# Optimization experiments

Measured on AMD Instinct MI355X. Metric: run time of the kernel, lower is better.

Reference implementation:

```python
import jax, jax.numpy as jnp
import numpy as np

H, N, L, B = 256, 64, 8192, 16   # d_model, d_state, l_max, batch
NH = N // 2                      # complex conjugate-pair halves (S4D convention)


def setup_inputs() -> dict:
    key = jax.random.key(0)
    ks = jax.random.split(key, 8)
    x = jax.random.normal(ks[0], (L, B, H), jnp.float32)
    # dt log-uniform in [1e-3, 1e-1] as in S4
    log_dt = jax.random.uniform(ks[1], (H,), jnp.float32) * (np.log(0.1) - np.log(0.001)) + np.log(0.001)
    # S4D-Lin initialization: A = -1/2 + i*pi*n
    A_real = jnp.log(0.5) * jnp.ones((H, NH), jnp.float32)            # log(-Re A)
    A_imag = np.pi * jnp.tile(jnp.arange(NH, dtype=jnp.float32), (H, 1))
    # 2 kernel channels for bidirectional
    C_real = jax.random.normal(ks[2], (2, H, NH), jnp.float32) * (0.5 ** 0.5)
    C_imag = jax.random.normal(ks[3], (2, H, NH), jnp.float32) * (0.5 ** 0.5)
    D = jax.random.normal(ks[4], (H,), jnp.float32)
    # position-wise output linear with GLU: H -> 2H, then glu over channel dim
    W_out = jax.random.normal(ks[5], (2 * H, H), jnp.float32) / np.sqrt(H)
    b_out = jnp.zeros((2 * H,), jnp.float32)
    return dict(x=x, log_dt=log_dt, A_real=A_real, A_imag=A_imag,
                C_real=C_real, C_imag=C_imag, D=D, W_out=W_out, b_out=b_out)


def _s4d_kernel(log_dt, A_real, A_imag, C_real, C_imag, length):
    """ZOH-discretized diagonal SSM kernel via Vandermonde. Returns (2, H, length) real."""
    dt = jnp.exp(log_dt)[:, None]                      # (H, 1)
    A = -jnp.exp(A_real) + 1j * A_imag                 # (H, NH)
    C = C_real + 1j * C_imag                           # (2, H, NH)
    dtA = A * dt                                       # (H, NH)
    Cd = C * (jnp.expm1(dtA) / A)                      # discretized C, (2, H, NH)
    # Vandermonde matrix exp(dtA * l) for l in [0, length)
    V = jnp.exp(dtA[:, :, None] * jnp.arange(length, dtype=jnp.float32))  # (H, NH, length)
    K = 2.0 * jnp.einsum('chn,hnl->chl', Cd, V).real   # (2, H, length)
    return K


def reference(x, log_dt, A_real, A_imag, C_real, C_imag, D, W_out, b_out):
    u = jnp.transpose(x, (1, 2, 0))                    # (B, H, L) -- TFTest transpose [1,2,0]
    Lq = u.shape[-1]
    n = 2 * Lq
    K = _s4d_kernel(log_dt, A_real, A_imag, C_real, C_imag, Lq)  # (2, H, L)
    # bidirectional: forward kernel padded right, flipped backward kernel padded left
    k = jnp.pad(K[0], ((0, 0), (0, Lq))) + jnp.pad(K[1][:, ::-1], ((0, 0), (Lq, 0)))  # (H, 2L)
    k_f = jnp.fft.rfft(k, n=n)                         # (H, n//2+1)
    u_f = jnp.fft.rfft(u, n=n)                         # (B, H, n//2+1)
    y = jnp.fft.irfft(u_f * k_f, n=n)[..., :Lq]        # (B, H, L)
    y = y + u * D[:, None]                             # skip connection
    y = jax.nn.gelu(y)
    z = jnp.einsum('oh,bhl->bol', W_out, y) + b_out[:, None]  # (B, 2H, L)
    out = z[:, :H] * jax.nn.sigmoid(z[:, H:])          # GLU over channel dim
    return out                                         # (B, H, L)
```

## Files before the change

kernel.cpp:

```cpp
#include <hip/hip_runtime.h>
#include <hip/hip_bf16.h>
#include <math.h>

#define HH  256
#define NHD 32
#define LL  8192
#define BB  16
#define HN  (HH*NHD)
#define BH  (BB*HH)
#define LC  256
#define NG  (LL/LC)
#define NINST (BB*NG)

typedef __attribute__((ext_vector_type(8))) short short8;
typedef __attribute__((ext_vector_type(4))) float floatx4;

__device__ __forceinline__ unsigned short f2bf(float f) {
  unsigned u = __float_as_uint(f);
  unsigned r = (u + 0x7FFF + ((u >> 16) & 1)) >> 16;
  return (unsigned short)r;
}
__device__ __forceinline__ float bf2f(unsigned short s) {
  return __uint_as_float((unsigned)s << 16);
}
__device__ __forceinline__ unsigned packbf2(float a, float b) {
  return (unsigned)f2bf(a) | ((unsigned)f2bf(b) << 16);
}
__device__ __forceinline__ float gelu_t(float y) {
  float y2 = y * y;
  float arg = 1.5957691216f * fmaf(0.044715f * y2, y, y);
  return y / (1.f + __expf(-arg));
}

__global__ void precomp_kernel(const float* __restrict__ log_dt,
                               const float* __restrict__ A_real,
                               const float* __restrict__ A_imag,
                               const float* __restrict__ C_real,
                               const float* __restrict__ C_imag,
                               float* __restrict__ P) {
  int i = blockIdx.x * blockDim.x + threadIdx.x;
  if (i >= HN) return;
  int h = i >> 5;
  double dt  = exp((double)log_dt[h]);
  double Are = -exp((double)A_real[i]);
  double Aim = (double)A_imag[i];
  double ar = Are * dt, ai = Aim * dt;
  double ea = exp(ar);
  double wr = ea * cos(ai), wi = ea * sin(ai);
  double em_r = wr - 1.0, em_i = wi;
  double den = Are * Are + Aim * Aim;
  double rr = (em_r * Are + em_i * Aim) / den;
  double ri = (em_i * Are - em_r * Aim) / den;
  P[0*HN + i] = (float)wr;
  P[1*HN + i] = (float)wi;
  {
    double cr = (double)C_real[i], ci = (double)C_imag[i];
    P[2*HN + i] = (float)(2.0 * (cr * rr - ci * ri));
    P[3*HN + i] = (float)(2.0 * (cr * ri + ci * rr));
  }
  {
    double cr = (double)C_real[HN + i], ci = (double)C_imag[HN + i];
    P[4*HN + i] = (float)(2.0 * (cr * rr - ci * ri));
    P[5*HN + i] = (float)(2.0 * (cr * ri + ci * rr));
  }
  {
    double arL = ar * (double)LC, aiL = ai * (double)LC;
    double eaL = exp(arL);
    P[6*HN + i] = (float)(eaL * cos(aiL));
    P[7*HN + i] = (float)(eaL * sin(aiL));
  }
  P[8*HN + i] = (float)ar;
  P[9*HN + i] = (float)ai;
}

__global__ __launch_bounds__(256) void wt_frag_kernel(const float* __restrict__ W,
                                                      unsigned short* __restrict__ Wf) {
  int og = blockIdx.x;
  #pragma unroll
  for (int i = 0; i < 2; ++i) {
    int j = i * 256 + threadIdx.x;
    int ks = j >> 6, ln = (j >> 2) & 15, lg = j & 3;
    const float* src = W + (size_t)(og * 16 + ln) * 256 + ks * 32 + lg * 8;
    short8 vv;
    #pragma unroll
    for (int e = 0; e < 8; ++e) vv[e] = (short)f2bf(src[e]);
    ((short8*)Wf)[og * 512 + j] = vv;
  }
}

__global__ __launch_bounds__(256) void kprep_kernel(const float* __restrict__ P,
                                                    float* __restrict__ Kf,
                                                    float* __restrict__ Kb) {
  int i = blockIdx.x * 256 + threadIdx.x;
  int d = i & 255, h = i >> 8;
  float fd = (float)d;
  float sf = 0.f, sb = 0.f;
  #pragma unroll 4
  for (int n = 0; n < NHD; ++n) {
    int j = h * NHD + n;
    float m  = __expf(fd * P[8*HN + j]);
    float ph = fd * P[9*HN + j];
    float cs = cosf(ph), sn = sinf(ph);
    float re = m * cs, im = m * sn;
    sf += P[2*HN + j] * re - P[3*HN + j] * im;
    sb += P[4*HN + j] * re - P[5*HN + j] * im;
  }
  Kf[i] = sf;
  Kb[i] = sb;
}

__global__ __launch_bounds__(256) void tprep_kernel(const float* __restrict__ Kf,
                                                    const float* __restrict__ Kb,
                                                    const float* __restrict__ Dv,
                                                    unsigned short* __restrict__ T) {
  int h = blockIdx.x, tt = blockIdx.y;
  const float* kf = Kf + h * 256;
  const float* kb = Kb + h * 256;
  float dh = Dv[h];
  short8* out = (short8*)T;
  #pragma unroll
  for (int i = 0; i < 2; ++i) {
    int j = i * 256 + threadIdx.x;
    int ks = j >> 6, ln = (j >> 2) & 15, lg = j & 3;
    int t = tt * 16 + ln;
    short8 vv;
    #pragma unroll
    for (int e = 0; e < 8; ++e) {
      int s = ks * 32 + lg * 8 + e;
      int d = t - s;
      float v = (d > 0) ? kf[d] : ((d < 0) ? kb[-d - 1] : (kf[0] + dh));
      vv[e] = (short)f2bf(v);
    }
    out[(size_t)(h * 16 + tt) * 512 + j] = vv;
  }
}

__global__ __launch_bounds__(256) void eprep_kernel(const float* __restrict__ P,
                                                    unsigned short* __restrict__ E) {
  int h = blockIdx.x, tt = blockIdx.y;
  int j = threadIdx.x;
  int ks = j >> 6, ln = (j >> 2) & 15, lg = j & 3;
  int t = tt * 16 + ln;
  int k0 = ks * 32 + lg * 8;
  short8 vv;
  if (k0 < 64) {
    float d = (float)(t + 1);
    #pragma unroll
    for (int q = 0; q < 4; ++q) {
      int n = (k0 >> 1) + q;
      int idx = h * NHD + n;
      float m  = __expf(d * P[8*HN + idx]);
      float ph = d * P[9*HN + idx];
      float re = m * cosf(ph), im = m * sinf(ph);
      float cr = P[2*HN + idx], ci = P[3*HN + idx];
      float zr = cr * re - ci * im;
      float zi = cr * im + ci * re;
      vv[2*q]   = (short)f2bf(zr);
      vv[2*q+1] = (short)f2bf(-zi);
    }
  } else {
    float d = (float)(LC - 1 - t);
    #pragma unroll
    for (int q = 0; q < 4; ++q) {
      int n = ((k0 - 64) >> 1) + q;
      int idx = h * NHD + n;
      float m  = __expf(d * P[8*HN + idx]);
      float ph = d * P[9*HN + idx];
      float re = m * cosf(ph), im = m * sinf(ph);
      float cr = P[4*HN + idx], ci = P[5*HN + idx];
      float zr = cr * re - ci * im;
      float zi = cr * im + ci * re;
      vv[2*q]   = (short)f2bf(zr);
      vv[2*q+1] = (short)f2bf(-zi);
    }
  }
  ((short8*)E)[(size_t)(h * 16 + tt) * 256 + j] = vv;
}

__global__ __launch_bounds__(256) void vprep_kernel(const float* __restrict__ P,
                                                    unsigned short* __restrict__ V) {
  int h = blockIdx.x, mt = blockIdx.y;
  #pragma unroll
  for (int i = 0; i < 2; ++i) {
    int j = i * 256 + threadIdx.x;
    int ks = j >> 6, ln = (j >> 2) & 15, lg = j & 3;
    int row = mt * 16 + ln;
    int dir = row >> 6, nc = row & 63;
    int n = nc >> 1, comp = nc & 1;
    int idx = h * NHD + n;
    float arn = P[8*HN + idx], ain = P[9*HN + idx];
    short8 vv;
    #pragma unroll
    for (int e = 0; e < 8; ++e) {
      int s = ks * 32 + lg * 8 + e;
      float d = (float)(dir ? s : (LC - 1 - s));
      float m = __expf(d * arn);
      float ph = d * ain;
      float v = m * (comp ? sinf(ph) : cosf(ph));
      vv[e] = (short)f2bf(v);
    }
    ((short8*)V)[(size_t)(h * 8 + mt) * 512 + j] = vv;
  }
}

__global__ __launch_bounds__(256) void transpose_kernel(const float* __restrict__ x,
                                                        unsigned short* __restrict__ UF) {
  __shared__ unsigned short tile[32][264];
  int b  = blockIdx.x;
  int lb = blockIdx.y * 32;
  int tid = threadIdx.x;
  int g = lb >> 8, ks = (lb & 255) >> 5;
  int inst = b * 32 + g, it = inst >> 4, lnw = inst & 15;
  #pragma unroll
  for (int i = 0; i < 8; ++i) {
    int idx = i * 256 + tid;
    int row = idx >> 6, c4 = idx & 63;
    float4 v = *(const float4*)(x + (size_t)(lb + row) * BH + b * 256 + c4 * 4);
    ushort4 u4v;
    u4v.x = f2bf(v.x); u4v.y = f2bf(v.y); u4v.z = f2bf(v.z); u4v.w = f2bf(v.w);
    *(ushort4*)&tile[row][c4 * 4] = u4v;
  }
  __syncthreads();
  short8* out = (short8*)UF;
  #pragma unroll
  for (int i = 0; i < 4; ++i) {
    int j = i * 256 + tid;
    int h = j >> 2, lg = j & 3;
    short8 vv;
    #pragma unroll
    for (int e = 0; e < 8; ++e) vv[e] = (short)tile[lg * 8 + e][h];
    out[(size_t)(h * 32 + it) * 512 + ks * 64 + lnw * 4 + lg] = vv;
  }
}

__device__ __forceinline__ void load_bu(const short8* __restrict__ U8, int h, int it,
                                        int ln, int lg, short8 (&Bf)[8]) {
  size_t ub = (size_t)(h * 32 + it) * 512 + ln * 4 + lg;
  #pragma unroll
  for (int ks = 0; ks < 8; ++ks) Bf[ks] = U8[ub + ks * 64];
}
__device__ __forceinline__ void load_bs(const short8* __restrict__ S8, int h, int it,
                                        int ln, int lg, short8 (&Sf)[4]) {
  size_t sb = (size_t)(h * 32 + it) * 256 + ln * 4 + lg;
  #pragma unroll
  for (int ks = 0; ks < 4; ++ks) Sf[ks] = S8[sb + ks * 64];
}

__global__ __launch_bounds__(512, 2) void sfin_mfma(const unsigned short* __restrict__ V,
                                                    const unsigned short* __restrict__ UF,
                                                    unsigned short* __restrict__ Sfin) {
  int tid = threadIdx.x, w = tid >> 6, lane = tid & 63;
  int ln = lane & 15, lg = lane >> 4;
  int h = blockIdx.x;
  const short8* U8 = (const short8*)UF;
  const short8* V8 = (const short8*)V;

  short8 Vf[8];
  size_t vb = (size_t)(h * 8 + w) * 512 + ln * 4 + lg;
  #pragma unroll
  for (int ks = 0; ks < 8; ++ks) Vf[ks] = V8[vb + ks * 64];

  short8 BfA[8], BfB[8];
  load_bu(U8, h, 0, ln, lg, BfA);

  for (int it = 0; it < 32; it += 2) {
    load_bu(U8, h, it + 1, ln, lg, BfB);
    {
      floatx4 acc = (floatx4){0.f, 0.f, 0.f, 0.f};
      #pragma unroll
      for (int ks = 0; ks < 8; ++ks)
        acc = __builtin_amdgcn_mfma_f32_16x16x32_bf16(Vf[ks], BfA[ks], acc, 0, 0, 0);
      unsigned short* sp = Sfin + ((size_t)h * NINST + it * 16 + ln) * 128 + w * 16 + lg * 4;
      uint2 pv; pv.x = packbf2(acc[0], acc[1]); pv.y = packbf2(acc[2], acc[3]);
      *(uint2*)sp = pv;
    }
    if (it + 2 < 32) load_bu(U8, h, it + 2, ln, lg, BfA);
    {
      floatx4 acc = (floatx4){0.f, 0.f, 0.f, 0.f};
      #pragma unroll
      for (int ks = 0; ks < 8; ++ks)
        acc = __builtin_amdgcn_mfma_f32_16x16x32_bf16(Vf[ks], BfB[ks], acc, 0, 0, 0);
      unsigned short* sp = Sfin + ((size_t)h * NINST + (it + 1) * 16 + ln) * 128 + w * 16 + lg * 4;
      uint2 pv; pv.x = packbf2(acc[0], acc[1]); pv.y = packbf2(acc[2], acc[3]);
      *(uint2*)sp = pv;
    }
  }
}

__global__ __launch_bounds__(256) void scanB_kernel(const float* __restrict__ P,
                                                    const unsigned short* __restrict__ Sfin,
                                                    unsigned short* __restrict__ Sc) {
  int t = blockIdx.x * 256 + threadIdx.x;
  if (t >= BH * NHD) return;
  int n = t & 31, h = (t >> 5) & 255, b = t >> 13;
  float wlr = P[6*HN + h*NHD + n], wli = P[7*HN + h*NHD + n];
  unsigned* sc = (unsigned*)Sc;
  {
    int k = 2 * n;
    int ks = k >> 5, lg = (k & 31) >> 3, eh = (k & 7) >> 1;
    float ar = 0.f, ai = 0.f;
    for (int g = 0; g < NG; ++g) {
      int inst = b * NG + g;
      int it = inst >> 4, ln = inst & 15;
      size_t chunk = (size_t)(h * 32 + it) * 256 + ks * 64 + ln * 4 + lg;
      sc[chunk * 4 + eh] = packbf2(ar, ai);
      const unsigned short* sp = Sfin + ((size_t)h * NINST + inst) * 128 + 2 * n;
      float lr = bf2f(sp[0]), li = bf2f(sp[1]);
      float nr = lr + wlr * ar - wli * ai;
      float ni = li + wlr * ai + wli * ar;
      ar = nr; ai = ni;
    }
  }
  {
    int k = 64 + 2 * n;
    int ks = k >> 5, lg = (k & 31) >> 3, eh = (k & 7) >> 1;
    float ar = 0.f, ai = 0.f;
    for (int g = NG - 1; g >= 0; --g) {
      int inst = b * NG + g;
      int it = inst >> 4, ln = inst & 15;
      size_t chunk = (size_t)(h * 32 + it) * 256 + ks * 64 + ln * 4 + lg;
      sc[chunk * 4 + eh] = packbf2(ar, ai);
      const unsigned short* sp = Sfin + ((size_t)h * NINST + inst) * 128 + 64 + 2 * n;
      float lr = bf2f(sp[0]), li = bf2f(sp[1]);
      float nr = lr + wlr * ar - wli * ai;
      float ni = li + wlr * ai + wli * ar;
      ar = nr; ai = ni;
    }
  }
}

__device__ __forceinline__ void comp_y(const short8 (&Tf)[2][8], const short8 (&Ef)[2][4],
                                       const short8 (&Bf)[8], const short8 (&Sf)[4],
                                       int h, int it, int w, int ln, int lg,
                                       unsigned short* __restrict__ Y2) {
  int inst = it * 16 + ln, bb = inst >> 5, g = inst & 31;
  unsigned short* yrow = Y2 + (size_t)(bb * 256 + h) * LL + g * 256;
  #pragma unroll
  for (int t2 = 0; t2 < 2; ++t2) {
    int tt = w * 2 + t2;
    floatx4 acc = (floatx4){0.f, 0.f, 0.f, 0.f};
    #pragma unroll
    for (int ks = 0; ks < 8; ++ks)
      acc = __builtin_amdgcn_mfma_f32_16x16x32_bf16(Tf[t2][ks], Bf[ks], acc, 0, 0, 0);
    #pragma unroll
    for (int ks = 0; ks < 4; ++ks)
      acc = __builtin_amdgcn_mfma_f32_16x16x32_bf16(Ef[t2][ks], Sf[ks], acc, 0, 0, 0);
    float y0 = gelu_t(acc[0]), y1 = gelu_t(acc[1]);
    float y2v = gelu_t(acc[2]), y3 = gelu_t(acc[3]);
    uint2 vv; vv.x = packbf2(y0, y1); vv.y = packbf2(y2v, y3);
    *(uint2*)(yrow + tt * 16 + lg * 4) = vv;
  }
}

__global__ __launch_bounds__(512, 2) void yloc_corr(const unsigned short* __restrict__ T,
                                                    const unsigned short* __restrict__ E,
                                                    const unsigned short* __restrict__ Sc,
                                                    const unsigned short* __restrict__ UF,
                                                    unsigned short* __restrict__ Y2) {
  int tid = threadIdx.x, w = tid >> 6, lane = tid & 63;
  int ln = lane & 15, lg = lane >> 4;
  int h = blockIdx.x;
  const short8* T8 = (const short8*)T;
  const short8* E8 = (const short8*)E;
  const short8* S8 = (const short8*)Sc;
  const short8* U8 = (const short8*)UF;

  short8 Tf[2][8], Ef[2][4];
  #pragma unroll
  for (int t2 = 0; t2 < 2; ++t2) {
    int tt = w * 2 + t2;
    size_t tb = (size_t)(h * 16 + tt) * 512 + ln * 4 + lg;
    #pragma unroll
    for (int ks = 0; ks < 8; ++ks) Tf[t2][ks] = T8[tb + ks * 64];
    size_t eb = (size_t)(h * 16 + tt) * 256 + ln * 4 + lg;
    #pragma unroll
    for (int ks = 0; ks < 4; ++ks) Ef[t2][ks] = E8[eb + ks * 64];
  }

  short8 BfA[8], SfA[4], BfB[8], SfB[4];
  load_bu(U8, h, 0, ln, lg, BfA);
  load_bs(S8, h, 0, ln, lg, SfA);

  for (int it = 0; it < 32; it += 2) {
    load_bu(U8, h, it + 1, ln, lg, BfB);
    load_bs(S8, h, it + 1, ln, lg, SfB);
    comp_y(Tf, Ef, BfA, SfA, h, it, w, ln, lg, Y2);
    if (it + 2 < 32) {
      load_bu(U8, h, it + 2, ln, lg, BfA);
      load_bs(S8, h, it + 2, ln, lg, SfA);
    }
    comp_y(Tf, Ef, BfB, SfB, h, it + 1, w, ln, lg, Y2);
  }
}

#define RAW_W 258
__global__ __launch_bounds__(512, 4) void gemm_mfma(
    const unsigned short* __restrict__ Wf,
    const unsigned short* __restrict__ Y2,
    const float* __restrict__ bvec, float* __restrict__ out) {
  __shared__ __align__(16) unsigned short ldsB[16384];
  __shared__ unsigned short raw[32 * RAW_W];
  int tid  = threadIdx.x;
  int w    = tid >> 6;
  int lane = tid & 63;
  int ln = lane & 15, lg = lane >> 4;
  int b  = blockIdx.x >> 7;
  int l0 = (blockIdx.x & 127) << 6;

  const short8* W8 = (const short8*)Wf;

  #pragma unroll
  for (int sl = 0; sl < 2; ++sl) {
    {
      int h = tid >> 1, lc = tid & 1;
      const unsigned short* src = Y2 + (((size_t)(b * 256 + h)) << 13) + l0 + sl * 32 + lc * 16;
      short8 v0 = ((const short8*)src)[0];
      short8 v1 = ((const short8*)src)[1];
      #pragma unroll
      for (int e = 0; e < 8; ++e) raw[(lc * 16 + e) * RAW_W + h] = (unsigned short)v0[e];
      #pragma unroll
      for (int e = 0; e < 8; ++e) raw[(lc * 16 + 8 + e) * RAW_W + h] = (unsigned short)v1[e];
    }
    __syncthreads();
    {
      int c = tid & 31, lq = tid >> 5;
      #pragma unroll
      for (int s2 = 0; s2 < 2; ++s2) {
        int lpp = lq + s2 * 16;
        int l = sl * 32 + lpp;
        short8 vv;
        #pragma unroll
        for (int e = 0; e < 8; ++e) vv[e] = (short)raw[lpp * RAW_W + c * 8 + e];
        ((short8*)ldsB)[l * 32 + (c ^ (l & 7))] = vv;
      }
    }
    __syncthreads();
  }

  floatx4 acc[4][4];
  #pragma unroll
  for (int m = 0; m < 4; ++m)
    #pragma unroll
    for (int n = 0; n < 4; ++n) acc[m][n] = (floatx4){0.f, 0.f, 0.f, 0.f};

  const short8* L8 = (const short8*)ldsB;
  #pragma unroll
  for (int ks = 0; ks < 8; ++ks) {
    short8 Bf[4];
    #pragma unroll
    for (int nf = 0; nf < 4; ++nf) {
      int row = nf * 16 + ln;
      Bf[nf] = L8[row * 32 + ((ks * 4 + lg) ^ (row & 7))];
    }
    #pragma unroll
    for (int mm = 0; mm < 4; ++mm) {
      int og = w * 2 + (mm & 1) + (mm >> 1) * 16;
      short8 Af = W8[(size_t)(og * 8 + ks) * 64 + ln * 4 + lg];
      #pragma unroll
      for (int nf = 0; nf < 4; ++nf)
        acc[mm][nf] = __builtin_amdgcn_mfma_f32_16x16x32_bf16(Af, Bf[nf], acc[mm][nf], 0, 0, 0);
    }
  }

  #pragma unroll
  for (int mm = 0; mm < 2; ++mm) {
    int obase = w * 32 + mm * 16 + lg * 4;
    #pragma unroll
    for (int r = 0; r < 4; ++r) {
      int o = obase + r;
      float b0 = bvec[o];
      float b1 = bvec[HH + o];
      float* op = out + ((size_t)(b * HH + o)) * LL + l0 + ln;
      #pragma unroll
      for (int nf = 0; nf < 4; ++nf) {
        float z1 = acc[mm][nf][r] + b0;
        float z2 = acc[mm + 2][nf][r] + b1;
        op[nf * 16] = z1 / (1.f + __expf(-z2));
      }
    }
  }
}

extern "C" void kernel_launch(void* const* d_in, const int* in_sizes, int n_in,
                              void* d_out, int out_size, void* d_ws, size_t ws_size,
                              hipStream_t stream) {
  const float* x      = (const float*)d_in[0];
  const float* log_dt = (const float*)d_in[1];
  const float* A_real = (const float*)d_in[2];
  const float* A_imag = (const float*)d_in[3];
  const float* C_real = (const float*)d_in[4];
  const float* C_imag = (const float*)d_in[5];
  const float* Dv     = (const float*)d_in[6];
  const float* W      = (const float*)d_in[7];
  const float* bvec   = (const float*)d_in[8];
  float* out = (float*)d_out;

  unsigned short* Sfin = (unsigned short*)d_out + 33554432;

  char* ws = (char*)d_ws;
  float*          P  = (float*)ws;
  unsigned short* Wf = (unsigned short*)(ws + 524288);
  float*          Kf = (float*)(ws + 786432);
  float*          Kb = (float*)(ws + 1048576);
  size_t OFF_UF = (size_t)2 << 20;
  size_t OFF_T  = OFF_UF + ((size_t)256 * 32 * 512 * 16);
  size_t OFF_E  = OFF_T + ((size_t)256 * 16 * 512 * 16);
  size_t OFF_V  = OFF_E + ((size_t)256 * 16 * 256 * 16);
  size_t OFF_SC = OFF_V + ((size_t)256 * 8 * 512 * 16);
  size_t OFF_Y2 = OFF_SC + ((size_t)256 * 32 * 256 * 16);
  unsigned short* UF = (unsigned short*)(ws + OFF_UF);
  unsigned short* T  = (unsigned short*)(ws + OFF_T);
  unsigned short* E  = (unsigned short*)(ws + OFF_E);
  unsigned short* V  = (unsigned short*)(ws + OFF_V);
  unsigned short* Sc = (unsigned short*)(ws + OFF_SC);
  unsigned short* Y2 = (unsigned short*)(ws + OFF_Y2);

  precomp_kernel<<<HN / 256, 256, 0, stream>>>(log_dt, A_real, A_imag, C_real, C_imag, P);
  wt_frag_kernel<<<32, 256, 0, stream>>>(W, Wf);
  kprep_kernel<<<HH * 256 / 256, 256, 0, stream>>>(P, Kf, Kb);
  tprep_kernel<<<dim3(HH, 16), 256, 0, stream>>>(Kf, Kb, Dv, T);
  eprep_kernel<<<dim3(HH, 16), 256, 0, stream>>>(P, E);
  vprep_kernel<<<dim3(HH, 8), 256, 0, stream>>>(P, V);
  transpose_kernel<<<dim3(BB, LL / 32), 256, 0, stream>>>(x, UF);
  sfin_mfma<<<HH, 512, 0, stream>>>(V, UF, Sfin);
  scanB_kernel<<<(BH * NHD) / 256, 256, 0, stream>>>(P, Sfin, Sc);
  yloc_corr<<<HH, 512, 0, stream>>>(T, E, Sc, UF, Y2);
  gemm_mfma<<<BB * (LL / 64), 512, 0, stream>>>(Wf, Y2, bvec, out);
}
```

Measured before the change: 293.1 us.

## Fuse chunk-state MFMA with inter-chunk scan via swizzled LDS

```diff
diff --git a/kernel.cpp b/kernel.cpp
--- a/kernel.cpp
+++ b/kernel.cpp
@@ -246,9 +246,11 @@
   for (int ks = 0; ks < 4; ++ks) Sf[ks] = S8[sb + ks * 64];
 }
 
-__global__ __launch_bounds__(512, 2) void sfin_mfma(const unsigned short* __restrict__ V,
+__global__ __launch_bounds__(512, 1) void sfin_scan(const unsigned short* __restrict__ V,
                                                     const unsigned short* __restrict__ UF,
-                                                    unsigned short* __restrict__ Sfin) {
+                                                    const float* __restrict__ P,
+                                                    unsigned short* __restrict__ Sc) {
+  __shared__ unsigned int SL[32768];
   int tid = threadIdx.x, w = tid >> 6, lane = tid & 63;
   int ln = lane & 15, lg = lane >> 4;
   int h = blockIdx.x;
@@ -260,52 +262,50 @@
   #pragma unroll
   for (int ks = 0; ks < 8; ++ks) Vf[ks] = V8[vb + ks * 64];
 
-  short8 BfA[8], BfB[8];
-  load_bu(U8, h, 0, ln, lg, BfA);
-
-  for (int it = 0; it < 32; it += 2) {
-    load_bu(U8, h, it + 1, ln, lg, BfB);
-    {
-      floatx4 acc = (floatx4){0.f, 0.f, 0.f, 0.f};
-      #pragma unroll
-      for (int ks = 0; ks < 8; ++ks)
-        acc = __builtin_amdgcn_mfma_f32_16x16x32_bf16(Vf[ks], BfA[ks], acc, 0, 0, 0);
-      unsigned short* sp = Sfin + ((size_t)h * NINST + it * 16 + ln) * 128 + w * 16 + lg * 4;
-      uint2 pv; pv.x = packbf2(acc[0], acc[1]); pv.y = packbf2(acc[2], acc[3]);
-      *(uint2*)sp = pv;
-    }
-    if (it + 2 < 32) load_bu(U8, h, it + 2, ln, lg, BfA);
-    {
-      floatx4 acc = (floatx4){0.f, 0.f, 0.f, 0.f};
-      #pragma unroll
-      for (int ks = 0; ks < 8; ++ks)
-        acc = __builtin_amdgcn_mfma_f32_16x16x32_bf16(Vf[ks], BfB[ks], acc, 0, 0, 0);
-      unsigned short* sp = Sfin + ((size_t)h * NINST + (it + 1) * 16 + ln) * 128 + w * 16 + lg * 4;
-      uint2 pv; pv.x = packbf2(acc[0], acc[1]); pv.y = packbf2(acc[2], acc[3]);
-      *(uint2*)sp = pv;
-    }
-  }
-}
-
-__global__ __launch_bounds__(256) void scanB_kernel(const float* __restrict__ P,
-                                                    const unsigned short* __restrict__ Sfin,
-                                                    unsigned short* __restrict__ Sc) {
-  int t = blockIdx.x * 256 + threadIdx.x;
-  if (t >= BH * NHD) return;
-  int n = t & 31, h = (t >> 5) & 255, b = t >> 13;
+  short8 B0[8], B1[8], B2[8], B3[8];
+  load_bu(U8, h, 0, ln, lg, B0);
+  load_bu(U8, h, 1, ln, lg, B1);
+  load_bu(U8, h, 2, ln, lg, B2);
+
+#define SFIN_STEP(BF, IT) { \
+    floatx4 acc = (floatx4){0.f, 0.f, 0.f, 0.f}; \
+    _Pragma("unroll") \
+    for (int ks = 0; ks < 8; ++ks) \
+      acc = __builtin_amdgcn_mfma_f32_16x16x32_bf16(Vf[ks], BF[ks], acc, 0, 0, 0); \
+    int inst = (IT) * 16 + ln; \
+    int kw = w * 8 + lg * 2; \
+    int word = inst * 64 + (kw ^ ((inst & 7) << 2)); \
+    uint2 pv; pv.x = packbf2(acc[0], acc[1]); pv.y = packbf2(acc[2], acc[3]); \
+    *(uint2*)&SL[word] = pv; }
+
+  for (int base = 0; base < 32; base += 4) {
+    if (base + 3 < 32) load_bu(U8, h, base + 3, ln, lg, B3);
+    SFIN_STEP(B0, base)
+    if (base + 4 < 32) load_bu(U8, h, base + 4, ln, lg, B0);
+    SFIN_STEP(B1, base + 1)
+    if (base + 5 < 32) load_bu(U8, h, base + 5, ln, lg, B1);
+    SFIN_STEP(B2, base + 2)
+    if (base + 6 < 32) load_bu(U8, h, base + 6, ln, lg, B2);
+    SFIN_STEP(B3, base + 3)
+  }
+#undef SFIN_STEP
+  __syncthreads();
+
+  int b = tid >> 5, n = tid & 31;
   float wlr = P[6*HN + h*NHD + n], wli = P[7*HN + h*NHD + n];
   unsigned* sc = (unsigned*)Sc;
   {
     int k = 2 * n;
-    int ks = k >> 5, lg = (k & 31) >> 3, eh = (k & 7) >> 1;
+    int ks = k >> 5, lgq = (k & 31) >> 3, eh = (k & 7) >> 1;
     float ar = 0.f, ai = 0.f;
     for (int g = 0; g < NG; ++g) {
       int inst = b * NG + g;
-      int it = inst >> 4, ln = inst & 15;
-      size_t chunk = (size_t)(h * 32 + it) * 256 + ks * 64 + ln * 4 + lg;
+      int it = inst >> 4, lnn = inst & 15;
+      size_t chunk = (size_t)(h * 32 + it) * 256 + ks * 64 + lnn * 4 + lgq;
       sc[chunk * 4 + eh] = packbf2(ar, ai);
-      const unsigned short* sp = Sfin + ((size_t)h * NINST + inst) * 128 + 2 * n;
-      float lr = bf2f(sp[0]), li = bf2f(sp[1]);
+      unsigned pv = SL[inst * 64 + (n ^ ((inst & 7) << 2))];
+      float lr = bf2f((unsigned short)(pv & 0xFFFF));
+      float li = bf2f((unsigned short)(pv >> 16));
       float nr = lr + wlr * ar - wli * ai;
       float ni = li + wlr * ai + wli * ar;
       ar = nr; ai = ni;
@@ -313,15 +313,16 @@
   }
   {
     int k = 64 + 2 * n;
-    int ks = k >> 5, lg = (k & 31) >> 3, eh = (k & 7) >> 1;
+    int ks = k >> 5, lgq = (k & 31) >> 3, eh = (k & 7) >> 1;
     float ar = 0.f, ai = 0.f;
     for (int g = NG - 1; g >= 0; --g) {
       int inst = b * NG + g;
-      int it = inst >> 4, ln = inst & 15;
-      size_t chunk = (size_t)(h * 32 + it) * 256 + ks * 64 + ln * 4 + lg;
+      int it = inst >> 4, lnn = inst & 15;
+      size_t chunk = (size_t)(h * 32 + it) * 256 + ks * 64 + lnn * 4 + lgq;
       sc[chunk * 4 + eh] = packbf2(ar, ai);
-      const unsigned short* sp = Sfin + ((size_t)h * NINST + inst) * 128 + 64 + 2 * n;
-      float lr = bf2f(sp[0]), li = bf2f(sp[1]);
+      unsigned pv = SL[inst * 64 + ((32 + n) ^ ((inst & 7) << 2))];
+      float lr = bf2f((unsigned short)(pv & 0xFFFF));
+      float li = bf2f((unsigned short)(pv >> 16));
       float nr = lr + wlr * ar - wli * ai;
       float ni = li + wlr * ai + wli * ar;
       ar = nr; ai = ni;
@@ -377,20 +378,21 @@
     for (int ks = 0; ks < 4; ++ks) Ef[t2][ks] = E8[eb + ks * 64];
   }
 
-  short8 BfA[8], SfA[4], BfB[8], SfB[4];
-  load_bu(U8, h, 0, ln, lg, BfA);
-  load_bs(S8, h, 0, ln, lg, SfA);
-
-  for (int it = 0; it < 32; it += 2) {
-    load_bu(U8, h, it + 1, ln, lg, BfB);
-    load_bs(S8, h, it + 1, ln, lg, SfB);
-    comp_y(Tf, Ef, BfA, SfA, h, it, w, ln, lg, Y2);
-    if (it + 2 < 32) {
-      load_bu(U8, h, it + 2, ln, lg, BfA);
-      load_bs(S8, h, it + 2, ln, lg, SfA);
-    }
-    comp_y(Tf, Ef, BfB, SfB, h, it + 1, w, ln, lg, Y2);
-  }
+  short8 B0[8], B1[8], B2[8];
+  short8 S0[4], S1[4], S2[4];
+  load_bu(U8, h, 0, ln, lg, B0); load_bs(S8, h, 0, ln, lg, S0);
+  load_bu(U8, h, 1, ln, lg, B1); load_bs(S8, h, 1, ln, lg, S1);
+
+  for (int base = 0; base < 30; base += 3) {
+    load_bu(U8, h, base + 2, ln, lg, B2); load_bs(S8, h, base + 2, ln, lg, S2);
+    comp_y(Tf, Ef, B0, S0, h, base, w, ln, lg, Y2);
+    load_bu(U8, h, base + 3, ln, lg, B0); load_bs(S8, h, base + 3, ln, lg, S0);
+    comp_y(Tf, Ef, B1, S1, h, base + 1, w, ln, lg, Y2);
+    if (base + 4 < 32) { load_bu(U8, h, base + 4, ln, lg, B1); load_bs(S8, h, base + 4, ln, lg, S1); }
+    comp_y(Tf, Ef, B2, S2, h, base + 2, w, ln, lg, Y2);
+  }
+  comp_y(Tf, Ef, B0, S0, h, 30, w, ln, lg, Y2);
+  comp_y(Tf, Ef, B1, S1, h, 31, w, ln, lg, Y2);
 }
 
 #define RAW_W 258
@@ -494,8 +496,6 @@
   const float* W      = (const float*)d_in[7];
   const float* bvec   = (const float*)d_in[8];
   float* out = (float*)d_out;
-
-  unsigned short* Sfin = (unsigned short*)d_out + 33554432;
 
   char* ws = (char*)d_ws;
   float*          P  = (float*)ws;
@@ -522,8 +522,7 @@
   eprep_kernel<<<dim3(HH, 16), 256, 0, stream>>>(P, E);
   vprep_kernel<<<dim3(HH, 8), 256, 0, stream>>>(P, V);
   transpose_kernel<<<dim3(BB, LL / 32), 256, 0, stream>>>(x, UF);
-  sfin_mfma<<<HH, 512, 0, stream>>>(V, UF, Sfin);
-  scanB_kernel<<<(BH * NHD) / 256, 256, 0, stream>>>(P, Sfin, Sc);
+  sfin_scan<<<HH, 512, 0, stream>>>(V, UF, P, Sc);
   yloc_corr<<<HH, 512, 0, stream>>>(T, E, Sc, UF, Y2);
   gemm_mfma<<<BB * (LL / 64), 512, 0, stream>>>(Wf, Y2, bvec, out);
 }
```

New measurement: 285.3 us. 1.03x faster.
